# Optimization experiments

Hardware: AMD Instinct MI355X
Metric: run time of the kernel (lower is better)

## Reference

```python
import jax, jax.numpy as jnp
import numpy as np
import math

B, N, D_IN, D = 64, 1024, 128, 128

def setup_inputs() -> dict:
    key = jax.random.key(0)
    ks = jax.random.split(key, 8)
    s_in = 1.0 / math.sqrt(D_IN)
    inp = {
        "x": jax.random.normal(ks[0], (B, N, D_IN), dtype=jnp.float32),
        "valid_lens": jax.random.randint(ks[1], (B,), 1, N + 1, dtype=jnp.int32),
        "Wq": jax.random.uniform(ks[2], (D_IN, D), jnp.float32, -s_in, s_in),
        "bq": jax.random.uniform(ks[3], (D,), jnp.float32, -s_in, s_in),
        "Wk": jax.random.uniform(ks[4], (D_IN, D), jnp.float32, -s_in, s_in),
        "bk": jax.random.uniform(ks[5], (D,), jnp.float32, -s_in, s_in),
        "Wv": jax.random.uniform(ks[6], (D_IN, D), jnp.float32, -s_in, s_in),
        "bv": jax.random.uniform(ks[7], (D,), jnp.float32, -s_in, s_in),
    }
    return inp

def reference(x, valid_lens, Wq, bq, Wk, bk, Wv, bv):
    # QKV projections
    q = x @ Wq + bq  # [B, N, D]
    k = x @ Wk + bk
    v = x @ Wv + bv
    scores = jnp.einsum("bnd,bmd->bnm", q, k) / math.sqrt(D)  # [B, N, N]
    # mask[b, i, j] = True where i >= valid_len[b] or j >= valid_len[b]
    idx = jnp.arange(N)
    invalid = idx[None, :] >= valid_lens[:, None]            # [B, N]
    mask = invalid[:, :, None] | invalid[:, None, :]          # [B, N, N]
    scores_masked = jnp.where(mask, jnp.float32(-1e12), scores)
    attn = jax.nn.softmax(scores_masked, axis=-1)
    attn = attn * (1.0 - mask.astype(attn.dtype))             # zero masked entries/rows
    return jnp.einsum("bnm,bmd->bnd", attn, v)
```

## Files before the change

kernel.cpp:

```cpp
#include <hip/hip_runtime.h>
#include <hip/hip_bf16.h>
#include <stdint.h>

#define B_ 64
#define N_ 1024
#define D_ 128

typedef __attribute__((ext_vector_type(8))) short bf16x8;
typedef __attribute__((ext_vector_type(4))) float f32x4;

__device__ __forceinline__ unsigned short f2bf(float f) {
    union { float f; uint32_t u; } v; v.f = f;
    uint32_t u = v.u;
    return (unsigned short)((u + 0x7FFFu + ((u >> 16) & 1u)) >> 16);
}

__global__ __launch_bounds__(256) void wtrans_kernel(
    const float* __restrict__ Wq, const float* __restrict__ Wk,
    const float* __restrict__ Wv, unsigned short* __restrict__ wt)
{
    int p = blockIdx.x >> 4;
    int seg = blockIdx.x & 15;
    const float* W = (p == 0) ? Wq : (p == 1) ? Wk : Wv;
    unsigned short* dst = wt + p * (D_ * D_);
    for (int i = 0; i < 4; ++i) {
        int idx = seg * 1024 + i * 256 + (int)threadIdx.x;
        int k = idx >> 7, d = idx & 127;
        dst[d * D_ + k] = f2bf(W[idx]);
    }
}

__global__ __launch_bounds__(256) void proj_kernel(
    const float* __restrict__ x,
    const unsigned short* __restrict__ wtg,
    const float* __restrict__ bq, const float* __restrict__ bk,
    const float* __restrict__ bv,
    unsigned short* __restrict__ qo, unsigned short* __restrict__ ko,
    unsigned short* __restrict__ vto)
{
    __shared__ alignas(16) unsigned short xs[64 * 136];
    __shared__ alignas(16) unsigned short ws[128 * 136];
    const int tid = threadIdx.x;
    const int row0 = blockIdx.x * 64;

    for (int it = 0; it < 8; ++it) {
        int idx4 = it * 256 + tid;
        int r = idx4 >> 5, c4 = (idx4 & 31) * 4;
        const float4 v = *(const float4*)&x[(size_t)(row0 + r) * D_ + c4];
        unsigned short tmp[4] = { f2bf(v.x), f2bf(v.y), f2bf(v.z), f2bf(v.w) };
        *(uint2*)&xs[r * 136 + c4] = *(uint2*)tmp;
    }

    const int wave = tid >> 6, lane = tid & 63;
    const int lr = lane & 15, lg = lane >> 4;
    const f32x4 zero4 = {0.f, 0.f, 0.f, 0.f};

    for (int p = 0; p < 3; ++p) {
        __syncthreads();
        const unsigned short* wsrc = wtg + p * (D_ * D_);
        for (int it = 0; it < 8; ++it) {
            int idx8 = it * 256 + tid;
            int r = idx8 >> 4, c8 = (idx8 & 15) * 8;
            *(bf16x8*)&ws[r * 136 + c8] = *(const bf16x8*)&wsrc[idx8 * 8];
        }
        __syncthreads();

        bf16x8 a[4];
        for (int kk = 0; kk < 4; ++kk)
            a[kk] = *(const bf16x8*)&xs[(wave * 16 + lr) * 136 + kk * 32 + lg * 8];
        f32x4 acc[8];
        for (int nt = 0; nt < 8; ++nt) acc[nt] = zero4;
        for (int kk = 0; kk < 4; ++kk)
            for (int nt = 0; nt < 8; ++nt) {
                bf16x8 bfr = *(const bf16x8*)&ws[(nt * 16 + lr) * 136 + kk * 32 + lg * 8];
                acc[nt] = __builtin_amdgcn_mfma_f32_16x16x32_bf16(a[kk], bfr, acc[nt], 0, 0, 0);
            }

        if (p < 2) {
            const float* bias = (p == 0) ? bq : bk;
            unsigned short* outp = (p == 0) ? qo : ko;
            const float sc = (p == 0) ? 0.08838834764831845f : 1.0f;
            for (int nt = 0; nt < 8; ++nt) {
                int d = nt * 16 + lr;
                float bb = bias[d];
                for (int r = 0; r < 4; ++r) {
                    int grow = row0 + wave * 16 + lg * 4 + r;
                    outp[(size_t)grow * D_ + d] = f2bf((acc[nt][r] + bb) * sc);
                }
            }
        } else {
            __syncthreads();
            for (int nt = 0; nt < 8; ++nt) {
                int d = nt * 16 + lr;
                float bb = bv[d];
                for (int r = 0; r < 4; ++r)
                    ws[d * 72 + wave * 16 + lg * 4 + r] = f2bf(acc[nt][r] + bb);
            }
            __syncthreads();
            const int b = row0 >> 10, n0 = row0 & 1023;
            unsigned short* dst = vto + ((size_t)b * D_) * N_ + n0;
            for (int it = 0; it < 4; ++it) {
                int idx = it * 256 + tid;
                int d = idx >> 3, c8 = (idx & 7) * 8;
                *(bf16x8*)&dst[(size_t)d * N_ + c8] = *(const bf16x8*)&ws[d * 72 + c8];
            }
        }
    }
}

__global__ __launch_bounds__(512, 2) void attn_kernel(
    const unsigned short* __restrict__ qg, const unsigned short* __restrict__ kg,
    const unsigned short* __restrict__ vtg, const int* __restrict__ valid_lens,
    float* __restrict__ out, int* __restrict__ ctr)
{
    __shared__ alignas(16) unsigned short smem[54272];
    __shared__ int slot;

    const int tid = threadIdx.x;
    const int wave = tid >> 6, lane = tid & 63;
    const int lr = lane & 15, lg = lane >> 4;
    const int grp = tid >> 8;
    const int wg = wave & 3;
    const int t256 = tid & 255;
    const int k_r = t256 >> 4, k_c = (t256 & 15) * 8;
    const int v_d = t256 >> 3, v_c = (t256 & 7) * 8;
    unsigned short* const ks_my = smem + grp * 8704;
    unsigned short* const vt_my = smem + 17408 + grp * 9216;
    unsigned short* const pw    = smem + 35840 + wave * 2304;
    float* const cmbO = (float*)smem;
    float* const cmbL = ((float*)smem) + 16640;
    const f32x4 zero4 = {0.f, 0.f, 0.f, 0.f};

    int item = blockIdx.x;
    while (item < 512) {
        const int qt = 7 - (item >> 6);
        const int b  = item & 63;
        const int L  = valid_lens[b];
        const int q0 = qt * 128;
        float* outb = out + ((size_t)b * N_ + q0) * D_;

        if (q0 >= L) {
            #pragma unroll
            for (int it = 0; it < 8; ++it) {
                int idx4 = it * 512 + tid;
                int r = idx4 >> 5, c4 = (idx4 & 31) * 4;
                float4 z; z.x = z.y = z.z = z.w = 0.f;
                *(float4*)&outb[(size_t)r * D_ + c4] = z;
            }
        } else {
            const int ntiles = (L + 63) >> 6;
            const int H = (ntiles + 1) >> 1;
            const int myStart = grp ? H : 0;
            const int myCnt = grp ? (ntiles - H) : H;
            const unsigned short* kgb = kg + (size_t)b * N_ * D_;
            const unsigned short* vtb = vtg + (size_t)b * D_ * N_;

            bf16x8 aq[2][4];
            #pragma unroll
            for (int rt = 0; rt < 2; ++rt) {
                const unsigned short* qrow =
                    qg + ((size_t)b * N_ + q0 + wg * 32 + rt * 16 + lr) * D_;
                #pragma unroll
                for (int kk = 0; kk < 4; ++kk)
                    aq[rt][kk] = *(const bf16x8*)&qrow[kk * 32 + lg * 8];
            }

            f32x4 oacc[2][8];
            #pragma unroll
            for (int rt = 0; rt < 2; ++rt)
                #pragma unroll
                for (int i = 0; i < 8; ++i) oacc[rt][i] = zero4;
            float lsum[2][4];
            #pragma unroll
            for (int rt = 0; rt < 2; ++rt)
                #pragma unroll
                for (int r = 0; r < 4; ++r) lsum[rt][r] = 0.f;

            bf16x8 kreg[4], vreg[4];

            if (myCnt > 0) {
                const int kv0 = myStart * 64;
                #pragma unroll
                for (int it = 0; it < 4; ++it)
                    kreg[it] = *(const bf16x8*)&kgb[(size_t)(kv0 + it * 16 + k_r) * D_ + k_c];
                #pragma unroll
                for (int it = 0; it < 4; ++it)
                    vreg[it] = *(const bf16x8*)&vtb[(size_t)(it * 32 + v_d) * N_ + kv0 + v_c];
                #pragma unroll
                for (int it = 0; it < 4; ++it)
                    *(bf16x8*)&ks_my[(it * 16 + k_r) * 136 + k_c] = kreg[it];
                #pragma unroll
                for (int it = 0; it < 4; ++it)
                    *(bf16x8*)&vt_my[(it * 32 + v_d) * 72 + v_c] = vreg[it];
            }
            __syncthreads();

            for (int r = 0; r < H; ++r) {
                const bool valid = (r < myCnt);
                const int t = myStart + r;
                const int kv0 = t * 64;

                if (r + 1 < myCnt) {
                    const int kvn = kv0 + 64;
                    #pragma unroll
                    for (int it = 0; it < 4; ++it)
                        kreg[it] = *(const bf16x8*)&kgb[(size_t)(kvn + it * 16 + k_r) * D_ + k_c];
                    #pragma unroll
                    for (int it = 0; it < 4; ++it)
                        vreg[it] = *(const bf16x8*)&vtb[(size_t)(it * 32 + v_d) * N_ + kvn + v_c];
                    __builtin_amdgcn_sched_barrier(0);
                }

                if (valid) {
                    f32x4 s[2][4];
                    #pragma unroll
                    for (int nt = 0; nt < 4; ++nt) {
                        s[0][nt] = zero4; s[1][nt] = zero4;
                        #pragma unroll
                        for (int kk = 0; kk < 4; ++kk) {
                            bf16x8 bk_ = *(const bf16x8*)&ks_my[(nt * 16 + lr) * 136 + kk * 32 + lg * 8];
                            s[0][nt] = __builtin_amdgcn_mfma_f32_16x16x32_bf16(aq[0][kk], bk_, s[0][nt], 0, 0, 0);
                            s[1][nt] = __builtin_amdgcn_mfma_f32_16x16x32_bf16(aq[1][kk], bk_, s[1][nt], 0, 0, 0);
                        }
                    }
                    #pragma unroll
                    for (int nt = 0; nt < 4; ++nt) {
                        const int j = kv0 + nt * 16 + lr;
                        const bool ok = (j < L);
                        #pragma unroll
                        for (int rt = 0; rt < 2; ++rt)
                            #pragma unroll
                            for (int r2 = 0; r2 < 4; ++r2) {
                                float e = ok ? __expf(s[rt][nt][r2]) : 0.f;
                                lsum[rt][r2] += e;
                                pw[(rt * 16 + lg * 4 + r2) * 72 + nt * 16 + lr] = f2bf(e);
                            }
                    }
                    #pragma unroll
                    for (int kk = 0; kk < 2; ++kk) {
                        bf16x8 ap0 = *(const bf16x8*)&pw[(0 * 16 + lr) * 72 + kk * 32 + lg * 8];
                        bf16x8 ap1 = *(const bf16x8*)&pw[(1 * 16 + lr) * 72 + kk * 32 + lg * 8];
                        #pragma unroll
                        for (int nt = 0; nt < 8; ++nt) {
                            bf16x8 bv_ = *(const bf16x8*)&vt_my[(nt * 16 + lr) * 72 + kk * 32 + lg * 8];
                            oacc[0][nt] = __builtin_amdgcn_mfma_f32_16x16x32_bf16(ap0, bv_, oacc[0][nt], 0, 0, 0);
                            oacc[1][nt] = __builtin_amdgcn_mfma_f32_16x16x32_bf16(ap1, bv_, oacc[1][nt], 0, 0, 0);
                        }
                    }
                }
                __syncthreads();
                if (r + 1 < myCnt) {
                    #pragma unroll
                    for (int it = 0; it < 4; ++it)
                        *(bf16x8*)&ks_my[(it * 16 + k_r) * 136 + k_c] = kreg[it];
                    #pragma unroll
                    for (int it = 0; it < 4; ++it)
                        *(bf16x8*)&vt_my[(it * 32 + v_d) * 72 + v_c] = vreg[it];
                }
                __syncthreads();
            }

            if (grp == 1) {
                #pragma unroll
                for (int rt = 0; rt < 2; ++rt)
                    #pragma unroll
                    for (int r2 = 0; r2 < 4; ++r2) {
                        float l = lsum[rt][r2];
                        #pragma unroll
                        for (int off = 1; off < 16; off <<= 1)
                            l += __shfl_xor(l, off);
                        const int row = wg * 32 + rt * 16 + lg * 4 + r2;
                        if (lr == 0) cmbL[row] = l;
                        #pragma unroll
                        for (int nt = 0; nt < 8; ++nt)
                            cmbO[row * 130 + nt * 16 + lr] = oacc[rt][nt][r2];
                    }
            }
            __syncthreads();
            if (grp == 0) {
                #pragma unroll
                for (int rt = 0; rt < 2; ++rt)
                    #pragma unroll
                    for (int r2 = 0; r2 < 4; ++r2) {
                        float l = lsum[rt][r2];
                        #pragma unroll
                        for (int off = 1; off < 16; off <<= 1)
                            l += __shfl_xor(l, off);
                        const int row = wg * 32 + rt * 16 + lg * 4 + r2;
                        l += cmbL[row];
                        const float inv = (q0 + row < L) ? 1.0f / l : 0.0f;
                        #pragma unroll
                        for (int nt = 0; nt < 8; ++nt) {
                            const int col = nt * 16 + lr;
                            outb[(size_t)row * D_ + col] =
                                (oacc[rt][nt][r2] + cmbO[row * 130 + col]) * inv;
                        }
                    }
            }
            __syncthreads();
        }

        if (tid == 0) slot = 256 + atomicAdd(ctr, 1);
        __syncthreads();
        item = slot;
        __syncthreads();
    }
}

extern "C" void kernel_launch(void* const* d_in, const int* in_sizes, int n_in,
                              void* d_out, int out_size, void* d_ws, size_t ws_size,
                              hipStream_t stream) {
    const float* x    = (const float*)d_in[0];
    const int*   vlen = (const int*)d_in[1];
    const float* Wq   = (const float*)d_in[2];
    const float* bq   = (const float*)d_in[3];
    const float* Wk   = (const float*)d_in[4];
    const float* bk   = (const float*)d_in[5];
    const float* Wv   = (const float*)d_in[6];
    const float* bv   = (const float*)d_in[7];
    float* out = (float*)d_out;

    unsigned short* wt  = (unsigned short*)d_ws;
    unsigned short* qws = (unsigned short*)((char*)d_ws + 98304);
    unsigned short* kws = qws + (size_t)B_ * N_ * D_;
    unsigned short* vtws = kws + (size_t)B_ * N_ * D_;
    int* ctr = (int*)((char*)d_ws + 98304 + 3 * (size_t)B_ * N_ * D_ * 2);

    hipMemsetAsync(ctr, 0, 4, stream);
    wtrans_kernel<<<48, 256, 0, stream>>>(Wq, Wk, Wv, wt);
    proj_kernel<<<(B_ * N_) / 64, 256, 0, stream>>>(x, wt, bq, bk, bv, qws, kws, vtws);
    attn_kernel<<<256, 512, 0, stream>>>(qws, kws, vtws, vlen, out, ctr);
}
```

Before: 74.13 us.

## Load V fragments straight from global to registers and transpose QK MFMA output layout

V^T tiles are no longer staged through shared memory. Each wave loads its MFMA B-operand fragments for V directly from global memory into registers, which cuts LDS footprint and LDS traffic but adds redundant global/L2 reads across waves and more register pressure. The QK^T MFMA operands are swapped so each lane holds four consecutive kv scores for one query row. This allows packed 8-byte P writes to LDS and a per-lane row sum that needs only two cross-group shuffles instead of a 16-lane reduction. Normalization is then redistributed with a single shuffle per output row.

```diff
diff --git a/kernel.cpp b/kernel.cpp
--- a/kernel.cpp
+++ b/kernel.cpp
@@ -113,7 +113,7 @@
     const unsigned short* __restrict__ vtg, const int* __restrict__ valid_lens,
     float* __restrict__ out, int* __restrict__ ctr)
 {
-    __shared__ alignas(16) unsigned short smem[54272];
+    __shared__ alignas(16) unsigned short smem[35840];
     __shared__ int slot;
 
     const int tid = threadIdx.x;
@@ -123,10 +123,8 @@
     const int wg = wave & 3;
     const int t256 = tid & 255;
     const int k_r = t256 >> 4, k_c = (t256 & 15) * 8;
-    const int v_d = t256 >> 3, v_c = (t256 & 7) * 8;
     unsigned short* const ks_my = smem + grp * 8704;
-    unsigned short* const vt_my = smem + 17408 + grp * 9216;
-    unsigned short* const pw    = smem + 35840 + wave * 2304;
+    unsigned short* const pw    = smem + 17408 + wave * 2304;
     float* const cmbO = (float*)smem;
     float* const cmbL = ((float*)smem) + 16640;
     const f32x4 zero4 = {0.f, 0.f, 0.f, 0.f};
@@ -170,13 +168,9 @@
             for (int rt = 0; rt < 2; ++rt)
                 #pragma unroll
                 for (int i = 0; i < 8; ++i) oacc[rt][i] = zero4;
-            float lsum[2][4];
-            #pragma unroll
-            for (int rt = 0; rt < 2; ++rt)
-                #pragma unroll
-                for (int r = 0; r < 4; ++r) lsum[rt][r] = 0.f;
-
-            bf16x8 kreg[4], vreg[4];
+            float lsum[2] = {0.f, 0.f};
+
+            bf16x8 kreg[4];
 
             if (myCnt > 0) {
                 const int kv0 = myStart * 64;
@@ -185,13 +179,7 @@
                     kreg[it] = *(const bf16x8*)&kgb[(size_t)(kv0 + it * 16 + k_r) * D_ + k_c];
                 #pragma unroll
                 for (int it = 0; it < 4; ++it)
-                    vreg[it] = *(const bf16x8*)&vtb[(size_t)(it * 32 + v_d) * N_ + kv0 + v_c];
-                #pragma unroll
-                for (int it = 0; it < 4; ++it)
                     *(bf16x8*)&ks_my[(it * 16 + k_r) * 136 + k_c] = kreg[it];
-                #pragma unroll
-                for (int it = 0; it < 4; ++it)
-                    *(bf16x8*)&vt_my[(it * 32 + v_d) * 72 + v_c] = vreg[it];
             }
             __syncthreads();
 
@@ -200,14 +188,21 @@
                 const int t = myStart + r;
                 const int kv0 = t * 64;
 
+                bf16x8 vf[16];
+                if (valid) {
+                    #pragma unroll
+                    for (int nt = 0; nt < 8; ++nt)
+                        #pragma unroll
+                        for (int kk = 0; kk < 2; ++kk)
+                            vf[nt * 2 + kk] = *(const bf16x8*)
+                                &vtb[(size_t)(nt * 16 + lr) * N_ + kv0 + kk * 32 + lg * 8];
+                    __builtin_amdgcn_sched_barrier(0);
+                }
                 if (r + 1 < myCnt) {
                     const int kvn = kv0 + 64;
                     #pragma unroll
                     for (int it = 0; it < 4; ++it)
                         kreg[it] = *(const bf16x8*)&kgb[(size_t)(kvn + it * 16 + k_r) * D_ + k_c];
-                    #pragma unroll
-                    for (int it = 0; it < 4; ++it)
-                        vreg[it] = *(const bf16x8*)&vtb[(size_t)(it * 32 + v_d) * N_ + kvn + v_c];
                     __builtin_amdgcn_sched_barrier(0);
                 }
 
@@ -219,22 +214,25 @@
                         #pragma unroll
                         for (int kk = 0; kk < 4; ++kk) {
                             bf16x8 bk_ = *(const bf16x8*)&ks_my[(nt * 16 + lr) * 136 + kk * 32 + lg * 8];
-                            s[0][nt] = __builtin_amdgcn_mfma_f32_16x16x32_bf16(aq[0][kk], bk_, s[0][nt], 0, 0, 0);
-                            s[1][nt] = __builtin_amdgcn_mfma_f32_16x16x32_bf16(aq[1][kk], bk_, s[1][nt], 0, 0, 0);
+                            s[0][nt] = __builtin_amdgcn_mfma_f32_16x16x32_bf16(bk_, aq[0][kk], s[0][nt], 0, 0, 0);
+                            s[1][nt] = __builtin_amdgcn_mfma_f32_16x16x32_bf16(bk_, aq[1][kk], s[1][nt], 0, 0, 0);
                         }
                     }
                     #pragma unroll
                     for (int nt = 0; nt < 4; ++nt) {
-                        const int j = kv0 + nt * 16 + lr;
-                        const bool ok = (j < L);
-                        #pragma unroll
-                        for (int rt = 0; rt < 2; ++rt)
-                            #pragma unroll
-                            for (int r2 = 0; r2 < 4; ++r2) {
-                                float e = ok ? __expf(s[rt][nt][r2]) : 0.f;
-                                lsum[rt][r2] += e;
-                                pw[(rt * 16 + lg * 4 + r2) * 72 + nt * 16 + lr] = f2bf(e);
-                            }
+                        const int kvb = kv0 + nt * 16 + lg * 4;
+                        #pragma unroll
+                        for (int rt = 0; rt < 2; ++rt) {
+                            float e0 = (kvb + 0 < L) ? __expf(s[rt][nt][0]) : 0.f;
+                            float e1 = (kvb + 1 < L) ? __expf(s[rt][nt][1]) : 0.f;
+                            float e2 = (kvb + 2 < L) ? __expf(s[rt][nt][2]) : 0.f;
+                            float e3 = (kvb + 3 < L) ? __expf(s[rt][nt][3]) : 0.f;
+                            lsum[rt] += (e0 + e1) + (e2 + e3);
+                            uint2 wv;
+                            wv.x = (uint32_t)f2bf(e0) | ((uint32_t)f2bf(e1) << 16);
+                            wv.y = (uint32_t)f2bf(e2) | ((uint32_t)f2bf(e3) << 16);
+                            *(uint2*)&pw[(rt * 16 + lr) * 72 + nt * 16 + lg * 4] = wv;
+                        }
                     }
                     #pragma unroll
                     for (int kk = 0; kk < 2; ++kk) {
@@ -242,9 +240,8 @@
                         bf16x8 ap1 = *(const bf16x8*)&pw[(1 * 16 + lr) * 72 + kk * 32 + lg * 8];
                         #pragma unroll
                         for (int nt = 0; nt < 8; ++nt) {
-                            bf16x8 bv_ = *(const bf16x8*)&vt_my[(nt * 16 + lr) * 72 + kk * 32 + lg * 8];
-                            oacc[0][nt] = __builtin_amdgcn_mfma_f32_16x16x32_bf16(ap0, bv_, oacc[0][nt], 0, 0, 0);
-                            oacc[1][nt] = __builtin_amdgcn_mfma_f32_16x16x32_bf16(ap1, bv_, oacc[1][nt], 0, 0, 0);
+                            oacc[0][nt] = __builtin_amdgcn_mfma_f32_16x16x32_bf16(ap0, vf[nt * 2 + kk], oacc[0][nt], 0, 0, 0);
+                            oacc[1][nt] = __builtin_amdgcn_mfma_f32_16x16x32_bf16(ap1, vf[nt * 2 + kk], oacc[1][nt], 0, 0, 0);
                         }
                     }
                 }
@@ -253,49 +250,50 @@
                     #pragma unroll
                     for (int it = 0; it < 4; ++it)
                         *(bf16x8*)&ks_my[(it * 16 + k_r) * 136 + k_c] = kreg[it];
-                    #pragma unroll
-                    for (int it = 0; it < 4; ++it)
-                        *(bf16x8*)&vt_my[(it * 32 + v_d) * 72 + v_c] = vreg[it];
                 }
                 __syncthreads();
             }
 
+            #pragma unroll
+            for (int rt = 0; rt < 2; ++rt) {
+                float l = lsum[rt];
+                l += __shfl_xor(l, 16);
+                l += __shfl_xor(l, 32);
+                lsum[rt] = l;
+            }
+
             if (grp == 1) {
                 #pragma unroll
-                for (int rt = 0; rt < 2; ++rt)
+                for (int rt = 0; rt < 2; ++rt) {
+                    if (lg == 0) cmbL[wg * 32 + rt * 16 + lr] = lsum[rt];
                     #pragma unroll
                     for (int r2 = 0; r2 < 4; ++r2) {
-                        float l = lsum[rt][r2];
-                        #pragma unroll
-                        for (int off = 1; off < 16; off <<= 1)
-                            l += __shfl_xor(l, off);
                         const int row = wg * 32 + rt * 16 + lg * 4 + r2;
-                        if (lr == 0) cmbL[row] = l;
                         #pragma unroll
                         for (int nt = 0; nt < 8; ++nt)
                             cmbO[row * 130 + nt * 16 + lr] = oacc[rt][nt][r2];
                     }
+                }
             }
             __syncthreads();
             if (grp == 0) {
                 #pragma unroll
-                for (int rt = 0; rt < 2; ++rt)
+                for (int rt = 0; rt < 2; ++rt) {
+                    const int qrow = q0 + wg * 32 + rt * 16 + lr;
+                    float tot = lsum[rt] + cmbL[wg * 32 + rt * 16 + lr];
+                    float invq = (qrow < L) ? 1.0f / tot : 0.0f;
                     #pragma unroll
                     for (int r2 = 0; r2 < 4; ++r2) {
-                        float l = lsum[rt][r2];
-                        #pragma unroll
-                        for (int off = 1; off < 16; off <<= 1)
-                            l += __shfl_xor(l, off);
+                        const float invr = __shfl(invq, lg * 4 + r2);
                         const int row = wg * 32 + rt * 16 + lg * 4 + r2;
-                        l += cmbL[row];
-                        const float inv = (q0 + row < L) ? 1.0f / l : 0.0f;
                         #pragma unroll
                         for (int nt = 0; nt < 8; ++nt) {
                             const int col = nt * 16 + lr;
                             outb[(size_t)row * D_ + col] =
-                                (oacc[rt][nt][r2] + cmbO[row * 130 + col]) * inv;
+                                (oacc[rt][nt][r2] + cmbO[row * 130 + col]) * invr;
                         }
                     }
+                }
             }
             __syncthreads();
         }
```

Result: slower. 97.49 us (+31.5%).
